# Kernel optimization log

Measured on AMD Instinct MI355X. Metric: run time of the kernel, lower is better.

The kernel has to match this reference:

```python
import jax, jax.numpy as jnp
import numpy as np

N = 50000   # n_nodes
E = 800000  # n_edges (avg degree 16)
D = 128     # d_model == hidden_dim
N_LAYERS = 3


def _xavier(key, fan_in, fan_out):
    limit = float(np.sqrt(6.0 / (fan_in + fan_out)))
    return jax.random.uniform(key, (fan_in, fan_out), jnp.float32, -limit, limit)


def setup_inputs() -> dict:
    key = jax.random.key(0)
    ks = jax.random.split(key, 2 + 2 * N_LAYERS)
    x = jax.random.normal(ks[0], (N, D), jnp.float32)
    edge_index = jax.random.randint(ks[1], (2, E), 0, N, jnp.int32)
    inp = {"x": x, "edge_index": edge_index}
    for i in range(N_LAYERS):
        inp[f"W{i}"] = _xavier(ks[2 + 2 * i], D, D)
        inp[f"b{i}"] = jax.random.uniform(ks[3 + 2 * i], (D,), jnp.float32, -0.1, 0.1)
    return inp


def _gcn_forward(x, src, dst, norm, Ws, bs):
    n = x.shape[0]
    h = x
    for i, (W, b) in enumerate(zip(Ws, bs)):
        m = (h @ W)[src] * norm[:, None]                       # [E+N, D] gather + scale
        h = jax.ops.segment_sum(m, dst, num_segments=n) + b    # scatter-add aggregate
        if i < len(Ws) - 1:
            h = jax.nn.relu(h)
    return h + x                                               # residual


def reference(x, edge_index, W0, b0, W1, b1, W2, b2):
    n = x.shape[0]
    loop = jnp.arange(n, dtype=edge_index.dtype)
    src = jnp.concatenate([edge_index[0], loop])  # add self-loops (GCNConv default)
    dst = jnp.concatenate([edge_index[1], loop])
    deg = jax.ops.segment_sum(jnp.ones_like(dst, x.dtype), dst, num_segments=n)
    dinv = jax.lax.rsqrt(deg)                     # deg >= 1 due to self-loops
    norm = dinv[src] * dinv[dst]                  # symmetric GCN normalization
    return _gcn_forward(x, src, dst, norm, (W0, W1, W2), (b0, b1, b2))
```

## Files before the change

kernel.cpp:

```cpp
#include <hip/hip_runtime.h>
#include <hip/hip_bf16.h>

#define D 128
#define BCAP 64
#define TM 64


__device__ __forceinline__ unsigned short f2bf_rtne(float f) {
    unsigned int u = __float_as_uint(f);
    u += 0x7fffu + ((u >> 16) & 1u);
    return (unsigned short)(u >> 16);
}

__device__ __forceinline__ float bf_lo(unsigned int u) { return __uint_as_float(u << 16); }
__device__ __forceinline__ float bf_hi(unsigned int u) { return __uint_as_float(u & 0xffff0000u); }


__device__ __forceinline__ void gemm_compute(const float* __restrict__ sh,
                                             const float* __restrict__ W,
                                             unsigned short* __restrict__ out,
                                             int n, int nbase) {
    const int tid = threadIdx.x;
    const int c4 = (tid & 31) << 2;
    const int ng = tid >> 5;
    const float* shb = &sh[(ng * 8) * D];

    float4 acc[8];
#pragma unroll
    for (int j = 0; j < 8; ++j) acc[j] = make_float4(0.f, 0.f, 0.f, 0.f);

    for (int k = 0; k < D; k += 4) {
        float4 w0 = *(const float4*)&W[(size_t)(k + 0) * D + c4];
        float4 w1 = *(const float4*)&W[(size_t)(k + 1) * D + c4];
        float4 w2 = *(const float4*)&W[(size_t)(k + 2) * D + c4];
        float4 w3 = *(const float4*)&W[(size_t)(k + 3) * D + c4];
#pragma unroll
        for (int j = 0; j < 8; ++j) {
            float4 hv = *(const float4*)&shb[j * D + k];
            acc[j].x = fmaf(hv.x, w0.x, acc[j].x); acc[j].y = fmaf(hv.x, w0.y, acc[j].y);
            acc[j].z = fmaf(hv.x, w0.z, acc[j].z); acc[j].w = fmaf(hv.x, w0.w, acc[j].w);
            acc[j].x = fmaf(hv.y, w1.x, acc[j].x); acc[j].y = fmaf(hv.y, w1.y, acc[j].y);
            acc[j].z = fmaf(hv.y, w1.z, acc[j].z); acc[j].w = fmaf(hv.y, w1.w, acc[j].w);
            acc[j].x = fmaf(hv.z, w2.x, acc[j].x); acc[j].y = fmaf(hv.z, w2.y, acc[j].y);
            acc[j].z = fmaf(hv.z, w2.z, acc[j].z); acc[j].w = fmaf(hv.z, w2.w, acc[j].w);
            acc[j].x = fmaf(hv.w, w3.x, acc[j].x); acc[j].y = fmaf(hv.w, w3.y, acc[j].y);
            acc[j].z = fmaf(hv.w, w3.z, acc[j].z); acc[j].w = fmaf(hv.w, w3.w, acc[j].w);
        }
    }

#pragma unroll
    for (int j = 0; j < 8; ++j) {
        int node = nbase + ng * 8 + j;
        if (node < n) {
            ushort4 p;
            p.x = f2bf_rtne(acc[j].x);
            p.y = f2bf_rtne(acc[j].y);
            p.z = f2bf_rtne(acc[j].z);
            p.w = f2bf_rtne(acc[j].w);
            *(ushort4*)&out[(size_t)node * D + c4] = p;
        }
    }
}


__global__ __launch_bounds__(256) void fused_gemm0_fill_kernel(
        const float* __restrict__ x, const float* __restrict__ W0,
        unsigned short* __restrict__ A,
        const int* __restrict__ src, const int* __restrict__ dst,
        int* __restrict__ cnt, unsigned short* __restrict__ bucket,
        int n, int E, int r, int gemmB, int fillB) {
    __shared__ float sh[TM * D];
    int b = blockIdx.x;
    if (b % r == 0) {
        int g = b / r;
        if (g >= gemmB) return;
        const int tid = threadIdx.x;
        const int nbase = g * TM;
#pragma unroll
        for (int i = 0; i < 8; ++i) {
            int fi = tid + i * 256;
            int node = nbase + (fi >> 5);
            float4 v = make_float4(0.f, 0.f, 0.f, 0.f);
            if (node < n) v = *(const float4*)&x[(size_t)node * D + ((fi & 31) << 2)];
            *(float4*)&sh[fi << 2] = v;
        }
        __syncthreads();
        gemm_compute(sh, W0, A, n, nbase);
    } else {
        int fid = b - b / r - 1;
        if (fid >= fillB) return;
        int e = fid * 256 + threadIdx.x;
        if (e >= E) return;
        int s = src[e];
        int d = dst[e];
        int pos = atomicAdd(&cnt[d], 1);
        if (pos < BCAP) bucket[((size_t)d << 6) + pos] = (unsigned short)s;
    }
}


__global__ __launch_bounds__(256) void gemm128_kernel(const unsigned short* __restrict__ h,
                                                      const float* __restrict__ W,
                                                      unsigned short* __restrict__ out, int n) {
    __shared__ float sh[TM * D];
    const int tid = threadIdx.x;
    const int nbase = blockIdx.x * TM;
#pragma unroll
    for (int i = 0; i < 8; ++i) {
        int fi = tid + i * 256;
        int node = nbase + (fi >> 5);
        float4 v = make_float4(0.f, 0.f, 0.f, 0.f);
        if (node < n) {
            ushort4 u = *(const ushort4*)&h[(size_t)node * D + ((fi & 31) << 2)];
            v.x = __uint_as_float((unsigned)u.x << 16);
            v.y = __uint_as_float((unsigned)u.y << 16);
            v.z = __uint_as_float((unsigned)u.z << 16);
            v.w = __uint_as_float((unsigned)u.w << 16);
        }
        *(float4*)&sh[fi << 2] = v;
    }
    __syncthreads();
    gemm_compute(sh, W, out, n, nbase);
}


__global__ __launch_bounds__(256) void gather_q_kernel(
        const int* __restrict__ cnt, const unsigned short* __restrict__ bucket,
        const unsigned short* __restrict__ hW, const float* __restrict__ bias,
        const float* __restrict__ x, float* __restrict__ out_f32,
        unsigned short* __restrict__ out_bf16, int n, int final_layer) {
    const int b = blockIdx.x;
    const int q = b & 3;
    const int tile = b >> 2;
    const int node = tile * 32 + (threadIdx.x >> 3);
    if (node >= n) return;
    const int fe = q * 32 + (threadIdx.x & 7) * 4;

    const unsigned short* row = bucket + ((size_t)node << 6);
    int len = cnt[node];
    float di = rsqrtf((float)len + 1.0f);
    if (len > BCAP) len = BCAP;
    const int len8 = len & ~7;

    float4 acc0 = make_float4(0.f, 0.f, 0.f, 0.f);
    float4 acc1 = make_float4(0.f, 0.f, 0.f, 0.f);
    int k = 0;
    for (; k < len8; k += 8) {
        uint4 pp = *(const uint4*)(row + k);
        int s0 = pp.x & 0xffff, s1 = pp.x >> 16;
        int s2 = pp.y & 0xffff, s3 = pp.y >> 16;
        int s4 = pp.z & 0xffff, s5 = pp.z >> 16;
        int s6 = pp.w & 0xffff, s7 = pp.w >> 16;
        float n0 = rsqrtf((float)cnt[s0] + 1.0f);
        float n1 = rsqrtf((float)cnt[s1] + 1.0f);
        float n2 = rsqrtf((float)cnt[s2] + 1.0f);
        float n3 = rsqrtf((float)cnt[s3] + 1.0f);
        float n4 = rsqrtf((float)cnt[s4] + 1.0f);
        float n5 = rsqrtf((float)cnt[s5] + 1.0f);
        float n6 = rsqrtf((float)cnt[s6] + 1.0f);
        float n7 = rsqrtf((float)cnt[s7] + 1.0f);
        uint2 u0 = *(const uint2*)&hW[(size_t)s0 * D + fe];
        uint2 u1 = *(const uint2*)&hW[(size_t)s1 * D + fe];
        uint2 u2 = *(const uint2*)&hW[(size_t)s2 * D + fe];
        uint2 u3 = *(const uint2*)&hW[(size_t)s3 * D + fe];
        uint2 u4 = *(const uint2*)&hW[(size_t)s4 * D + fe];
        uint2 u5 = *(const uint2*)&hW[(size_t)s5 * D + fe];
        uint2 u6 = *(const uint2*)&hW[(size_t)s6 * D + fe];
        uint2 u7 = *(const uint2*)&hW[(size_t)s7 * D + fe];
        acc0.x = fmaf(bf_lo(u0.x), n0, acc0.x); acc0.y = fmaf(bf_hi(u0.x), n0, acc0.y);
        acc0.z = fmaf(bf_lo(u0.y), n0, acc0.z); acc0.w = fmaf(bf_hi(u0.y), n0, acc0.w);
        acc1.x = fmaf(bf_lo(u1.x), n1, acc1.x); acc1.y = fmaf(bf_hi(u1.x), n1, acc1.y);
        acc1.z = fmaf(bf_lo(u1.y), n1, acc1.z); acc1.w = fmaf(bf_hi(u1.y), n1, acc1.w);
        acc0.x = fmaf(bf_lo(u2.x), n2, acc0.x); acc0.y = fmaf(bf_hi(u2.x), n2, acc0.y);
        acc0.z = fmaf(bf_lo(u2.y), n2, acc0.z); acc0.w = fmaf(bf_hi(u2.y), n2, acc0.w);
        acc1.x = fmaf(bf_lo(u3.x), n3, acc1.x); acc1.y = fmaf(bf_hi(u3.x), n3, acc1.y);
        acc1.z = fmaf(bf_lo(u3.y), n3, acc1.z); acc1.w = fmaf(bf_hi(u3.y), n3, acc1.w);
        acc0.x = fmaf(bf_lo(u4.x), n4, acc0.x); acc0.y = fmaf(bf_hi(u4.x), n4, acc0.y);
        acc0.z = fmaf(bf_lo(u4.y), n4, acc0.z); acc0.w = fmaf(bf_hi(u4.y), n4, acc0.w);
        acc1.x = fmaf(bf_lo(u5.x), n5, acc1.x); acc1.y = fmaf(bf_hi(u5.x), n5, acc1.y);
        acc1.z = fmaf(bf_lo(u5.y), n5, acc1.z); acc1.w = fmaf(bf_hi(u5.y), n5, acc1.w);
        acc0.x = fmaf(bf_lo(u6.x), n6, acc0.x); acc0.y = fmaf(bf_hi(u6.x), n6, acc0.y);
        acc0.z = fmaf(bf_lo(u6.y), n6, acc0.z); acc0.w = fmaf(bf_hi(u6.y), n6, acc0.w);
        acc1.x = fmaf(bf_lo(u7.x), n7, acc1.x); acc1.y = fmaf(bf_hi(u7.x), n7, acc1.y);
        acc1.z = fmaf(bf_lo(u7.y), n7, acc1.z); acc1.w = fmaf(bf_hi(u7.y), n7, acc1.w);
    }
    for (; k < len; ++k) {
        int s = row[k];
        float ns = rsqrtf((float)cnt[s] + 1.0f);
        uint2 u = *(const uint2*)&hW[(size_t)s * D + fe];
        acc0.x = fmaf(bf_lo(u.x), ns, acc0.x); acc0.y = fmaf(bf_hi(u.x), ns, acc0.y);
        acc0.z = fmaf(bf_lo(u.y), ns, acc0.z); acc0.w = fmaf(bf_hi(u.y), ns, acc0.w);
    }

    uint2 uh = *(const uint2*)&hW[(size_t)node * D + fe];
    float4 acc;
    acc.x = fmaf(bf_lo(uh.x), di, acc0.x + acc1.x);
    acc.y = fmaf(bf_hi(uh.x), di, acc0.y + acc1.y);
    acc.z = fmaf(bf_lo(uh.y), di, acc0.z + acc1.z);
    acc.w = fmaf(bf_hi(uh.y), di, acc0.w + acc1.w);

    float4 bv = *(const float4*)&bias[fe];
    float4 r;
    r.x = fmaf(acc.x, di, bv.x);
    r.y = fmaf(acc.y, di, bv.y);
    r.z = fmaf(acc.z, di, bv.z);
    r.w = fmaf(acc.w, di, bv.w);

    if (final_layer) {
        float4 xv = *(const float4*)&x[(size_t)node * D + fe];
        r.x += xv.x; r.y += xv.y; r.z += xv.z; r.w += xv.w;
        *(float4*)&out_f32[(size_t)node * D + fe] = r;
    } else {
        ushort4 p;
        p.x = f2bf_rtne(fmaxf(r.x, 0.f));
        p.y = f2bf_rtne(fmaxf(r.y, 0.f));
        p.z = f2bf_rtne(fmaxf(r.z, 0.f));
        p.w = f2bf_rtne(fmaxf(r.w, 0.f));
        *(ushort4*)&out_bf16[(size_t)node * D + fe] = p;
    }
}


extern "C" void kernel_launch(void* const* d_in, const int* in_sizes, int n_in,
                              void* d_out, int out_size, void* d_ws, size_t ws_size,
                              hipStream_t stream) {
    const float* x  = (const float*)d_in[0];
    const int*   ei = (const int*)d_in[1];
    const float* Ws[3] = {(const float*)d_in[2], (const float*)d_in[4], (const float*)d_in[6]};
    const float* bs[3] = {(const float*)d_in[3], (const float*)d_in[5], (const float*)d_in[7]};
    float* out = (float*)d_out;

    const int N = in_sizes[0] / D;
    const int E = in_sizes[1] / 2;
    const int* src = ei;
    const int* dst = ei + E;

    char* wsb = (char*)d_ws;
    size_t off = 0;
    int* cnt = (int*)(wsb + off);               off += (size_t)N * sizeof(int);
    off = (off + 255) & ~(size_t)255;
    unsigned short* bucket = (unsigned short*)(wsb + off);  off += (size_t)N * BCAP * 2;
    off = (off + 255) & ~(size_t)255;
    unsigned short* A  = (unsigned short*)(wsb + off);      off += (size_t)N * D * 2;
    off = (off + 255) & ~(size_t)255;
    unsigned short* B  = (unsigned short*)(wsb + off);

    const int gemmB = (N + TM - 1) / TM;
    const int fillB = (E + 255) / 256;
    const int r = 1 + (fillB + gemmB - 1) / gemmB;
    const int fusedGrid = gemmB * r;
    const int gatherGrid = ((N + 31) / 32) * 4;

    hipMemsetAsync(cnt, 0, (size_t)N * sizeof(int), stream);
    fused_gemm0_fill_kernel<<<fusedGrid, 256, 0, stream>>>(x, Ws[0], A, src, dst,
                                                           cnt, bucket, N, E, r, gemmB, fillB);
    gather_q_kernel<<<gatherGrid, 256, 0, stream>>>(cnt, bucket, A, bs[0], x, out, B, N, 0);
    gemm128_kernel<<<gemmB, 256, 0, stream>>>(B, Ws[1], A, N);
    gather_q_kernel<<<gatherGrid, 256, 0, stream>>>(cnt, bucket, A, bs[1], x, out, B, N, 0);
    gemm128_kernel<<<gemmB, 256, 0, stream>>>(B, Ws[2], A, N);
    gather_q_kernel<<<gatherGrid, 256, 0, stream>>>(cnt, bucket, A, bs[2], x, out, B, N, 1);
}
```

Before: 370.3 us.

## Pre-scale GEMM outputs by source degree norm and widen gather to full rows

Layers 1 and 2 now fold the source-side rsqrt(deg) factor into the GEMM epilogue, so their gathers no longer load cnt[s] per edge or compute rsqrt. The first gather still uses per-edge norms because the fused GEMM0 runs alongside the degree fill and cannot know degrees yet. The gather mapping also changes from four feature-quarter blocks per 32-node tile to one 32-thread group covering all 128 features of a node. This removes the random cnt lookups and duplicated index reads, at the cost of an extra rounding step when the scaled values are stored as bf16.

```diff
diff --git a/kernel.cpp b/kernel.cpp
--- a/kernel.cpp
+++ b/kernel.cpp
@@ -19,6 +19,7 @@
 __device__ __forceinline__ void gemm_compute(const float* __restrict__ sh,
                                              const float* __restrict__ W,
                                              unsigned short* __restrict__ out,
+                                             const int* __restrict__ cnt,
                                              int n, int nbase) {
     const int tid = threadIdx.x;
     const int c4 = (tid & 31) << 2;
@@ -52,11 +53,13 @@
     for (int j = 0; j < 8; ++j) {
         int node = nbase + ng * 8 + j;
         if (node < n) {
+            float sc = 1.0f;
+            if (cnt) sc = rsqrtf((float)cnt[node] + 1.0f);
             ushort4 p;
-            p.x = f2bf_rtne(acc[j].x);
-            p.y = f2bf_rtne(acc[j].y);
-            p.z = f2bf_rtne(acc[j].z);
-            p.w = f2bf_rtne(acc[j].w);
+            p.x = f2bf_rtne(acc[j].x * sc);
+            p.y = f2bf_rtne(acc[j].y * sc);
+            p.z = f2bf_rtne(acc[j].z * sc);
+            p.w = f2bf_rtne(acc[j].w * sc);
             *(ushort4*)&out[(size_t)node * D + c4] = p;
         }
     }
@@ -85,7 +88,7 @@
             *(float4*)&sh[fi << 2] = v;
         }
         __syncthreads();
-        gemm_compute(sh, W0, A, n, nbase);
+        gemm_compute(sh, W0, A, nullptr, n, nbase);
     } else {
         int fid = b - b / r - 1;
         if (fid >= fillB) return;
@@ -99,9 +102,9 @@
 }
 
 
-__global__ __launch_bounds__(256) void gemm128_kernel(const unsigned short* __restrict__ h,
-                                                      const float* __restrict__ W,
-                                                      unsigned short* __restrict__ out, int n) {
+__global__ __launch_bounds__(256) void gemm128_scaled_kernel(
+        const unsigned short* __restrict__ h, const float* __restrict__ W,
+        unsigned short* __restrict__ out, const int* __restrict__ cnt, int n) {
     __shared__ float sh[TM * D];
     const int tid = threadIdx.x;
     const int nbase = blockIdx.x * TM;
@@ -120,22 +123,18 @@
         *(float4*)&sh[fi << 2] = v;
     }
     __syncthreads();
-    gemm_compute(sh, W, out, n, nbase);
-}
-
-
-__global__ __launch_bounds__(256) void gather_q_kernel(
+    gemm_compute(sh, W, out, cnt, n, nbase);
+}
+
+
+__global__ __launch_bounds__(256) void gather_kernel(
         const int* __restrict__ cnt, const unsigned short* __restrict__ bucket,
         const unsigned short* __restrict__ hW, const float* __restrict__ bias,
         const float* __restrict__ x, float* __restrict__ out_f32,
-        unsigned short* __restrict__ out_bf16, int n, int final_layer) {
-    const int b = blockIdx.x;
-    const int q = b & 3;
-    const int tile = b >> 2;
-    const int node = tile * 32 + (threadIdx.x >> 3);
+        unsigned short* __restrict__ out_bf16, int n, int scaled_in, int final_layer) {
+    int node = blockIdx.x * 8 + (threadIdx.x >> 5);
     if (node >= n) return;
-    const int fe = q * 32 + (threadIdx.x & 7) * 4;
-
+    const int f = (threadIdx.x & 31) << 2;
     const unsigned short* row = bucket + ((size_t)node << 6);
     int len = cnt[node];
     float di = rsqrtf((float)len + 1.0f);
@@ -145,61 +144,93 @@
     float4 acc0 = make_float4(0.f, 0.f, 0.f, 0.f);
     float4 acc1 = make_float4(0.f, 0.f, 0.f, 0.f);
     int k = 0;
-    for (; k < len8; k += 8) {
-        uint4 pp = *(const uint4*)(row + k);
-        int s0 = pp.x & 0xffff, s1 = pp.x >> 16;
-        int s2 = pp.y & 0xffff, s3 = pp.y >> 16;
-        int s4 = pp.z & 0xffff, s5 = pp.z >> 16;
-        int s6 = pp.w & 0xffff, s7 = pp.w >> 16;
-        float n0 = rsqrtf((float)cnt[s0] + 1.0f);
-        float n1 = rsqrtf((float)cnt[s1] + 1.0f);
-        float n2 = rsqrtf((float)cnt[s2] + 1.0f);
-        float n3 = rsqrtf((float)cnt[s3] + 1.0f);
-        float n4 = rsqrtf((float)cnt[s4] + 1.0f);
-        float n5 = rsqrtf((float)cnt[s5] + 1.0f);
-        float n6 = rsqrtf((float)cnt[s6] + 1.0f);
-        float n7 = rsqrtf((float)cnt[s7] + 1.0f);
-        uint2 u0 = *(const uint2*)&hW[(size_t)s0 * D + fe];
-        uint2 u1 = *(const uint2*)&hW[(size_t)s1 * D + fe];
-        uint2 u2 = *(const uint2*)&hW[(size_t)s2 * D + fe];
-        uint2 u3 = *(const uint2*)&hW[(size_t)s3 * D + fe];
-        uint2 u4 = *(const uint2*)&hW[(size_t)s4 * D + fe];
-        uint2 u5 = *(const uint2*)&hW[(size_t)s5 * D + fe];
-        uint2 u6 = *(const uint2*)&hW[(size_t)s6 * D + fe];
-        uint2 u7 = *(const uint2*)&hW[(size_t)s7 * D + fe];
-        acc0.x = fmaf(bf_lo(u0.x), n0, acc0.x); acc0.y = fmaf(bf_hi(u0.x), n0, acc0.y);
-        acc0.z = fmaf(bf_lo(u0.y), n0, acc0.z); acc0.w = fmaf(bf_hi(u0.y), n0, acc0.w);
-        acc1.x = fmaf(bf_lo(u1.x), n1, acc1.x); acc1.y = fmaf(bf_hi(u1.x), n1, acc1.y);
-        acc1.z = fmaf(bf_lo(u1.y), n1, acc1.z); acc1.w = fmaf(bf_hi(u1.y), n1, acc1.w);
-        acc0.x = fmaf(bf_lo(u2.x), n2, acc0.x); acc0.y = fmaf(bf_hi(u2.x), n2, acc0.y);
-        acc0.z = fmaf(bf_lo(u2.y), n2, acc0.z); acc0.w = fmaf(bf_hi(u2.y), n2, acc0.w);
-        acc1.x = fmaf(bf_lo(u3.x), n3, acc1.x); acc1.y = fmaf(bf_hi(u3.x), n3, acc1.y);
-        acc1.z = fmaf(bf_lo(u3.y), n3, acc1.z); acc1.w = fmaf(bf_hi(u3.y), n3, acc1.w);
-        acc0.x = fmaf(bf_lo(u4.x), n4, acc0.x); acc0.y = fmaf(bf_hi(u4.x), n4, acc0.y);
-        acc0.z = fmaf(bf_lo(u4.y), n4, acc0.z); acc0.w = fmaf(bf_hi(u4.y), n4, acc0.w);
-        acc1.x = fmaf(bf_lo(u5.x), n5, acc1.x); acc1.y = fmaf(bf_hi(u5.x), n5, acc1.y);
-        acc1.z = fmaf(bf_lo(u5.y), n5, acc1.z); acc1.w = fmaf(bf_hi(u5.y), n5, acc1.w);
-        acc0.x = fmaf(bf_lo(u6.x), n6, acc0.x); acc0.y = fmaf(bf_hi(u6.x), n6, acc0.y);
-        acc0.z = fmaf(bf_lo(u6.y), n6, acc0.z); acc0.w = fmaf(bf_hi(u6.y), n6, acc0.w);
-        acc1.x = fmaf(bf_lo(u7.x), n7, acc1.x); acc1.y = fmaf(bf_hi(u7.x), n7, acc1.y);
-        acc1.z = fmaf(bf_lo(u7.y), n7, acc1.z); acc1.w = fmaf(bf_hi(u7.y), n7, acc1.w);
-    }
-    for (; k < len; ++k) {
-        int s = row[k];
-        float ns = rsqrtf((float)cnt[s] + 1.0f);
-        uint2 u = *(const uint2*)&hW[(size_t)s * D + fe];
-        acc0.x = fmaf(bf_lo(u.x), ns, acc0.x); acc0.y = fmaf(bf_hi(u.x), ns, acc0.y);
-        acc0.z = fmaf(bf_lo(u.y), ns, acc0.z); acc0.w = fmaf(bf_hi(u.y), ns, acc0.w);
-    }
-
-    uint2 uh = *(const uint2*)&hW[(size_t)node * D + fe];
+    if (scaled_in) {
+        for (; k < len8; k += 8) {
+            uint4 pp = *(const uint4*)(row + k);
+            int s0 = pp.x & 0xffff, s1 = pp.x >> 16;
+            int s2 = pp.y & 0xffff, s3 = pp.y >> 16;
+            int s4 = pp.z & 0xffff, s5 = pp.z >> 16;
+            int s6 = pp.w & 0xffff, s7 = pp.w >> 16;
+            uint2 u0 = *(const uint2*)&hW[(size_t)s0 * D + f];
+            uint2 u1 = *(const uint2*)&hW[(size_t)s1 * D + f];
+            uint2 u2 = *(const uint2*)&hW[(size_t)s2 * D + f];
+            uint2 u3 = *(const uint2*)&hW[(size_t)s3 * D + f];
+            uint2 u4 = *(const uint2*)&hW[(size_t)s4 * D + f];
+            uint2 u5 = *(const uint2*)&hW[(size_t)s5 * D + f];
+            uint2 u6 = *(const uint2*)&hW[(size_t)s6 * D + f];
+            uint2 u7 = *(const uint2*)&hW[(size_t)s7 * D + f];
+            acc0.x += bf_lo(u0.x); acc0.y += bf_hi(u0.x); acc0.z += bf_lo(u0.y); acc0.w += bf_hi(u0.y);
+            acc1.x += bf_lo(u1.x); acc1.y += bf_hi(u1.x); acc1.z += bf_lo(u1.y); acc1.w += bf_hi(u1.y);
+            acc0.x += bf_lo(u2.x); acc0.y += bf_hi(u2.x); acc0.z += bf_lo(u2.y); acc0.w += bf_hi(u2.y);
+            acc1.x += bf_lo(u3.x); acc1.y += bf_hi(u3.x); acc1.z += bf_lo(u3.y); acc1.w += bf_hi(u3.y);
+            acc0.x += bf_lo(u4.x); acc0.y += bf_hi(u4.x); acc0.z += bf_lo(u4.y); acc0.w += bf_hi(u4.y);
+            acc1.x += bf_lo(u5.x); acc1.y += bf_hi(u5.x); acc1.z += bf_lo(u5.y); acc1.w += bf_hi(u5.y);
+            acc0.x += bf_lo(u6.x); acc0.y += bf_hi(u6.x); acc0.z += bf_lo(u6.y); acc0.w += bf_hi(u6.y);
+            acc1.x += bf_lo(u7.x); acc1.y += bf_hi(u7.x); acc1.z += bf_lo(u7.y); acc1.w += bf_hi(u7.y);
+        }
+        for (; k < len; ++k) {
+            int s = row[k];
+            uint2 u = *(const uint2*)&hW[(size_t)s * D + f];
+            acc0.x += bf_lo(u.x); acc0.y += bf_hi(u.x); acc0.z += bf_lo(u.y); acc0.w += bf_hi(u.y);
+        }
+    } else {
+        for (; k < len8; k += 8) {
+            uint4 pp = *(const uint4*)(row + k);
+            int s0 = pp.x & 0xffff, s1 = pp.x >> 16;
+            int s2 = pp.y & 0xffff, s3 = pp.y >> 16;
+            int s4 = pp.z & 0xffff, s5 = pp.z >> 16;
+            int s6 = pp.w & 0xffff, s7 = pp.w >> 16;
+            float n0 = rsqrtf((float)cnt[s0] + 1.0f);
+            float n1 = rsqrtf((float)cnt[s1] + 1.0f);
+            float n2 = rsqrtf((float)cnt[s2] + 1.0f);
+            float n3 = rsqrtf((float)cnt[s3] + 1.0f);
+            float n4 = rsqrtf((float)cnt[s4] + 1.0f);
+            float n5 = rsqrtf((float)cnt[s5] + 1.0f);
+            float n6 = rsqrtf((float)cnt[s6] + 1.0f);
+            float n7 = rsqrtf((float)cnt[s7] + 1.0f);
+            uint2 u0 = *(const uint2*)&hW[(size_t)s0 * D + f];
+            uint2 u1 = *(const uint2*)&hW[(size_t)s1 * D + f];
+            uint2 u2 = *(const uint2*)&hW[(size_t)s2 * D + f];
+            uint2 u3 = *(const uint2*)&hW[(size_t)s3 * D + f];
+            uint2 u4 = *(const uint2*)&hW[(size_t)s4 * D + f];
+            uint2 u5 = *(const uint2*)&hW[(size_t)s5 * D + f];
+            uint2 u6 = *(const uint2*)&hW[(size_t)s6 * D + f];
+            uint2 u7 = *(const uint2*)&hW[(size_t)s7 * D + f];
+            acc0.x = fmaf(bf_lo(u0.x), n0, acc0.x); acc0.y = fmaf(bf_hi(u0.x), n0, acc0.y);
+            acc0.z = fmaf(bf_lo(u0.y), n0, acc0.z); acc0.w = fmaf(bf_hi(u0.y), n0, acc0.w);
+            acc1.x = fmaf(bf_lo(u1.x), n1, acc1.x); acc1.y = fmaf(bf_hi(u1.x), n1, acc1.y);
+            acc1.z = fmaf(bf_lo(u1.y), n1, acc1.z); acc1.w = fmaf(bf_hi(u1.y), n1, acc1.w);
+            acc0.x = fmaf(bf_lo(u2.x), n2, acc0.x); acc0.y = fmaf(bf_hi(u2.x), n2, acc0.y);
+            acc0.z = fmaf(bf_lo(u2.y), n2, acc0.z); acc0.w = fmaf(bf_hi(u2.y), n2, acc0.w);
+            acc1.x = fmaf(bf_lo(u3.x), n3, acc1.x); acc1.y = fmaf(bf_hi(u3.x), n3, acc1.y);
+            acc1.z = fmaf(bf_lo(u3.y), n3, acc1.z); acc1.w = fmaf(bf_hi(u3.y), n3, acc1.w);
+            acc0.x = fmaf(bf_lo(u4.x), n4, acc0.x); acc0.y = fmaf(bf_hi(u4.x), n4, acc0.y);
+            acc0.z = fmaf(bf_lo(u4.y), n4, acc0.z); acc0.w = fmaf(bf_hi(u4.y), n4, acc0.w);
+            acc1.x = fmaf(bf_lo(u5.x), n5, acc1.x); acc1.y = fmaf(bf_hi(u5.x), n5, acc1.y);
+            acc1.z = fmaf(bf_lo(u5.y), n5, acc1.z); acc1.w = fmaf(bf_hi(u5.y), n5, acc1.w);
+            acc0.x = fmaf(bf_lo(u6.x), n6, acc0.x); acc0.y = fmaf(bf_hi(u6.x), n6, acc0.y);
+            acc0.z = fmaf(bf_lo(u6.y), n6, acc0.z); acc0.w = fmaf(bf_hi(u6.y), n6, acc0.w);
+            acc1.x = fmaf(bf_lo(u7.x), n7, acc1.x); acc1.y = fmaf(bf_hi(u7.x), n7, acc1.y);
+            acc1.z = fmaf(bf_lo(u7.y), n7, acc1.z); acc1.w = fmaf(bf_hi(u7.y), n7, acc1.w);
+        }
+        for (; k < len; ++k) {
+            int s = row[k];
+            float ns = rsqrtf((float)cnt[s] + 1.0f);
+            uint2 u = *(const uint2*)&hW[(size_t)s * D + f];
+            acc0.x = fmaf(bf_lo(u.x), ns, acc0.x); acc0.y = fmaf(bf_hi(u.x), ns, acc0.y);
+            acc0.z = fmaf(bf_lo(u.y), ns, acc0.z); acc0.w = fmaf(bf_hi(u.y), ns, acc0.w);
+        }
+    }
+
+    uint2 uh = *(const uint2*)&hW[(size_t)node * D + f];
+    float sf = scaled_in ? 1.0f : di;
     float4 acc;
-    acc.x = fmaf(bf_lo(uh.x), di, acc0.x + acc1.x);
-    acc.y = fmaf(bf_hi(uh.x), di, acc0.y + acc1.y);
-    acc.z = fmaf(bf_lo(uh.y), di, acc0.z + acc1.z);
-    acc.w = fmaf(bf_hi(uh.y), di, acc0.w + acc1.w);
-
-    float4 bv = *(const float4*)&bias[fe];
+    acc.x = fmaf(bf_lo(uh.x), sf, acc0.x + acc1.x);
+    acc.y = fmaf(bf_hi(uh.x), sf, acc0.y + acc1.y);
+    acc.z = fmaf(bf_lo(uh.y), sf, acc0.z + acc1.z);
+    acc.w = fmaf(bf_hi(uh.y), sf, acc0.w + acc1.w);
+
+    float4 bv = *(const float4*)&bias[f];
     float4 r;
     r.x = fmaf(acc.x, di, bv.x);
     r.y = fmaf(acc.y, di, bv.y);
@@ -207,16 +238,16 @@
     r.w = fmaf(acc.w, di, bv.w);
 
     if (final_layer) {
-        float4 xv = *(const float4*)&x[(size_t)node * D + fe];
+        float4 xv = *(const float4*)&x[(size_t)node * D + f];
         r.x += xv.x; r.y += xv.y; r.z += xv.z; r.w += xv.w;
-        *(float4*)&out_f32[(size_t)node * D + fe] = r;
+        *(float4*)&out_f32[(size_t)node * D + f] = r;
     } else {
         ushort4 p;
         p.x = f2bf_rtne(fmaxf(r.x, 0.f));
         p.y = f2bf_rtne(fmaxf(r.y, 0.f));
         p.z = f2bf_rtne(fmaxf(r.z, 0.f));
         p.w = f2bf_rtne(fmaxf(r.w, 0.f));
-        *(ushort4*)&out_bf16[(size_t)node * D + fe] = p;
+        *(ushort4*)&out_bf16[(size_t)node * D + f] = p;
     }
 }
 
@@ -249,14 +280,14 @@
     const int fillB = (E + 255) / 256;
     const int r = 1 + (fillB + gemmB - 1) / gemmB;
     const int fusedGrid = gemmB * r;
-    const int gatherGrid = ((N + 31) / 32) * 4;
+    const int gatherGrid = (N + 7) / 8;
 
     hipMemsetAsync(cnt, 0, (size_t)N * sizeof(int), stream);
     fused_gemm0_fill_kernel<<<fusedGrid, 256, 0, stream>>>(x, Ws[0], A, src, dst,
                                                            cnt, bucket, N, E, r, gemmB, fillB);
-    gather_q_kernel<<<gatherGrid, 256, 0, stream>>>(cnt, bucket, A, bs[0], x, out, B, N, 0);
-    gemm128_kernel<<<gemmB, 256, 0, stream>>>(B, Ws[1], A, N);
-    gather_q_kernel<<<gatherGrid, 256, 0, stream>>>(cnt, bucket, A, bs[1], x, out, B, N, 0);
-    gemm128_kernel<<<gemmB, 256, 0, stream>>>(B, Ws[2], A, N);
-    gather_q_kernel<<<gatherGrid, 256, 0, stream>>>(cnt, bucket, A, bs[2], x, out, B, N, 1);
-}
+    gather_kernel<<<gatherGrid, 256, 0, stream>>>(cnt, bucket, A, bs[0], x, out, B, N, 0, 0);
+    gemm128_scaled_kernel<<<gemmB, 256, 0, stream>>>(B, Ws[1], A, cnt, N);
+    gather_kernel<<<gatherGrid, 256, 0, stream>>>(cnt, bucket, A, bs[1], x, out, B, N, 1, 0);
+    gemm128_scaled_kernel<<<gemmB, 256, 0, stream>>>(B, Ws[2], A, cnt, N);
+    gather_kernel<<<gatherGrid, 256, 0, stream>>>(cnt, bucket, A, bs[2], x, out, B, N, 1, 1);
+}
```

Result: faster. 319.6 us (-13.7%).
